# Kernel tuning notes

Measured on AMD Instinct MI355X. Metric: run time of the kernel, lower is better.

## Reference

```python
import jax, jax.numpy as jnp
import numpy as np

D_MODEL = 1024
N_HEADS = 16
D_HEAD = D_MODEL // N_HEADS
RANK = 16
DECAY = 0.95
ALPHA_MAX = 0.05
BETA = 0.01


def setup_inputs() -> dict:
    key = jax.random.key(0)
    ks = jax.random.split(key, 9)
    B, T = 4, 2048
    s = 0.02  # init scale for weights
    return {
        "hidden_states": jax.random.normal(ks[0], (B, T, D_MODEL), jnp.float32),
        "m_gate": jax.random.uniform(ks[1], (B, T), jnp.float32),
        "alpha_scale": jax.random.uniform(ks[2], (B, T, N_HEADS), jnp.float32),
        "Wq": jax.random.normal(ks[3], (D_MODEL, D_MODEL), jnp.float32) * s,
        "Wk": jax.random.normal(ks[4], (D_MODEL, D_MODEL), jnp.float32) * s,
        "Wv": jax.random.normal(ks[5], (D_MODEL, D_MODEL), jnp.float32) * s,
        "Wo": jax.random.normal(ks[6], (D_MODEL, D_MODEL), jnp.float32) * s,
        "Wa": jax.random.normal(ks[7], (N_HEADS, D_MODEL), jnp.float32) * s,
        "ba": jnp.zeros((N_HEADS,), jnp.float32),
        "mix_logit": jnp.zeros((N_HEADS,), jnp.float32),
    }


def reference(hidden_states, m_gate, alpha_scale, Wq, Wk, Wv, Wo, Wa, ba, mix_logit):
    B, T, D = hidden_states.shape
    H, Dh, R = N_HEADS, D_HEAD, RANK
    # batched projections (Linear: x @ W.T), then split heads
    q = (hidden_states @ Wq.T).reshape(B, T, H, Dh)
    k = (hidden_states @ Wk.T).reshape(B, T, H, Dh)
    v = (hidden_states @ Wv.T).reshape(B, T, H, Dh)
    # alpha computed under torch.no_grad in the original -> stop_gradient
    alpha = jax.nn.sigmoid(hidden_states @ Wa.T + ba)  # [B,T,H]
    alpha = alpha * m_gate[..., None] * alpha_scale
    alpha = jnp.minimum(alpha, ALPHA_MAX)
    alpha = jax.lax.stop_gradient(alpha)

    inv_sqrt_dh = 1.0 / (Dh ** 0.5)

    def step(carry, xs):
        U, V = carry  # U: [B,H,Dh,R], V: [B,H,R,Dh]
        q_t, k_t, v_t, a_t = xs  # [B,H,Dh], [B,H,Dh], [B,H,Dh], [B,H]
        U = DECAY * U
        V = DECAY * V
        ku = jnp.einsum('bhd,bhdr->bhr', k_t, U)
        a = a_t[..., None, None]
        U = U + a * jnp.einsum('bhd,bhr->bhdr', k_t, ku)
        V = V + a * jnp.einsum('bhr,bhd->bhrd', ku, v_t)
        U = U - BETA * jnp.clip(U, -1.0, 1.0)
        V = V - BETA * jnp.clip(V, -1.0, 1.0)
        # whole fast-weight update is no_grad in the original
        U = jax.lax.stop_gradient(U)
        V = jax.lax.stop_gradient(V)
        q_norm = q_t * inv_sqrt_dh
        k_fast = jnp.einsum('bhdr,bhrd->bhd', U, V)  # [B,H,Dh]
        score_slow = jnp.sum(q_norm * k_t, axis=-1)  # [B,H]
        score_fast = jnp.sum(q_norm * k_fast, axis=-1)
        logits = jnp.stack([score_slow, score_fast], axis=-1) + mix_logit[None, :, None]
        mix = jax.nn.softmax(logits, axis=-1)  # [B,H,2]
        y = mix[..., 0:1] * v_t + mix[..., 1:2] * k_fast  # [B,H,Dh]
        return (U, V), y

    U0 = jnp.zeros((B, H, Dh, R), hidden_states.dtype)
    V0 = jnp.zeros((B, H, R, Dh), hidden_states.dtype)
    xs = (jnp.moveaxis(q, 1, 0), jnp.moveaxis(k, 1, 0),
          jnp.moveaxis(v, 1, 0), jnp.moveaxis(alpha, 1, 0))
    _, ys = jax.lax.scan(step, (U0, V0), xs)  # ys: [T,B,H,Dh]
    y = jnp.moveaxis(ys, 0, 1).reshape(B, T, D)
    return y @ Wo.T
```

## Files before the change

kernel.cpp:

```cpp
#include <hip/hip_runtime.h>
#include <hip/hip_bf16.h>
#include <stdint.h>

#define D_MODEL 1024
#define N_HEADS 16
#define D_HEAD  64
#define SEQ_T   2048
#define BATCH   4

typedef unsigned short u16;
typedef __bf16 bf16x8 __attribute__((ext_vector_type(8)));
typedef float  f32x4  __attribute__((ext_vector_type(4)));

#define NT 32
#define BUF 4096

__device__ __forceinline__ u16 f2bf(float x) {
  unsigned u = __float_as_uint(x);
  u += 0x7fffu + ((u >> 16) & 1u);
  return (u16)(u >> 16);
}
__device__ __forceinline__ unsigned pk2(float a, float b) {
  return (unsigned)f2bf(a) | ((unsigned)f2bf(b) << 16);
}
__device__ __forceinline__ unsigned scale2(unsigned p, float s) {
  float lo = __uint_as_float(p << 16) * s;
  float hi = __uint_as_float(p & 0xffff0000u) * s;
  return pk2(lo, hi);
}
__device__ __forceinline__ void cp16(const u16* g, u16* l) {
  __builtin_amdgcn_global_load_lds(
      (const __attribute__((address_space(1))) unsigned int*)g,
      (__attribute__((address_space(3))) unsigned int*)l, 16, 0, 0);
}

__global__ __launch_bounds__(256) void cast_kernel(const float* __restrict__ hs,
                                                   const float* __restrict__ wq,
                                                   const float* __restrict__ wk,
                                                   const float* __restrict__ wv,
                                                   const float* __restrict__ wo,
                                                   u16* __restrict__ Xb,
                                                   u16* __restrict__ Wb) {
  int g = blockIdx.x * 256 + threadIdx.x;
  const float4* src; uint4* dst;
  if (g < (1 << 20)) {
    src = (const float4*)hs + 2 * (size_t)g;
    dst = (uint4*)Xb + g;
  } else {
    int j = g - (1 << 20);
    int R = j >> 7;
    int col8 = j & 127;
    const float* s;
    int srow;
    if (R < 2048) {
      int h = R >> 7, c = R & 127, jj = c >> 4, l = c & 15;
      srow = h * 64 + (jj >> 1) * 16 + l;
      s = (jj & 1) ? wk : wq;
    } else if (R < 3072) { s = wv; srow = R - 2048; }
    else                 { s = wo; srow = R - 3072; }
    src = (const float4*)s + (size_t)srow * 256 + col8 * 2;
    dst = (uint4*)Wb + (size_t)R * 128 + col8;
  }
  float4 lo = src[0], hi = src[1];
  uint4 o;
  o.x = pk2(lo.x, lo.y); o.y = pk2(lo.z, lo.w);
  o.z = pk2(hi.x, hi.y); o.w = pk2(hi.z, hi.w);
  *dst = o;
}

__global__ __launch_bounds__(256, 4) void gemm_qkv_kernel(const u16* __restrict__ A,
                                                          const u16* __restrict__ B,
                                                          u16* __restrict__ Vb,
                                                          float* __restrict__ S) {
  constexpr int K = D_MODEL;
  __shared__ u16 As[2 * BUF];
  __shared__ u16 Bs[2 * BUF];
  const int tid  = threadIdx.x;
  const int lane = tid & 63;
  const int wave = tid >> 6;
  const int wm = (wave >> 1) * 64;
  const int wn = (wave & 1) * 64;
  const int bm = blockIdx.y * 128;
  const int bn = blockIdx.x;
  const int quad = lane >> 4;
  const int l16  = lane & 15;
  const int rchunk = quad ^ ((l16 >> 1) & 3);

  const int lr = tid >> 2;
  const int lch = tid & 3;
  const int wch = lch ^ ((lr >> 1) & 3);
  const u16* Ap0 = A + (size_t)(bm + lr) * K + lch * 8;
  const u16* Ap1 = Ap0 + (size_t)64 * K;
  const u16* Bp0 = B + (size_t)(bn * 128 + lr) * K + lch * 8;
  const u16* Bp1 = Bp0 + (size_t)64 * K;
  u16* Aw0 = As + lr * 32 + wch * 8;
  u16* Aw1 = Aw0 + 64 * 32;
  u16* Bw0 = Bs + lr * 32 + wch * 8;
  u16* Bw1 = Bw0 + 64 * 32;

  f32x4 acc[4][4];
  #pragma unroll
  for (int i = 0; i < 4; ++i)
    #pragma unroll
    for (int j = 0; j < 4; ++j) acc[i][j] = (f32x4){0.f, 0.f, 0.f, 0.f};

  uint4 a0 = *(const uint4*)Ap0;
  uint4 a1 = *(const uint4*)Ap1;
  uint4 b0 = *(const uint4*)Bp0;
  uint4 b1 = *(const uint4*)Bp1;
  *(uint4*)Aw0 = a0; *(uint4*)Aw1 = a1;
  *(uint4*)Bw0 = b0; *(uint4*)Bw1 = b1;
  a0 = *(const uint4*)(Ap0 + 32);
  a1 = *(const uint4*)(Ap1 + 32);
  b0 = *(const uint4*)(Bp0 + 32);
  b1 = *(const uint4*)(Bp1 + 32);
  __syncthreads();

  #pragma unroll 2
  for (int t = 0; t < NT; ++t) {
    const int p = t & 1;
    const u16* Ar = As + p * BUF;
    const u16* Br = Bs + p * BUF;
    bf16x8 af[4], bfr[4];
    #pragma unroll
    for (int i = 0; i < 4; ++i)
      af[i] = *(const bf16x8*)(Ar + (wm + i * 16 + l16) * 32 + rchunk * 8);
    #pragma unroll
    for (int j = 0; j < 4; ++j)
      bfr[j] = *(const bf16x8*)(Br + (wn + j * 16 + l16) * 32 + rchunk * 8);
    if (t + 1 < NT) {
      const int q = (p ^ 1) * BUF;
      *(uint4*)(Aw0 + q) = a0; *(uint4*)(Aw1 + q) = a1;
      *(uint4*)(Bw0 + q) = b0; *(uint4*)(Bw1 + q) = b1;
      if (t + 2 < NT) {
        const int o = (t + 2) * 32;
        a0 = *(const uint4*)(Ap0 + o);
        a1 = *(const uint4*)(Ap1 + o);
        b0 = *(const uint4*)(Bp0 + o);
        b1 = *(const uint4*)(Bp1 + o);
      }
    }
    #pragma unroll
    for (int i = 0; i < 4; ++i)
      #pragma unroll
      for (int j = 0; j < 4; ++j)
        acc[i][j] = __builtin_amdgcn_mfma_f32_16x16x32_bf16(af[i], bfr[j], acc[i][j], 0, 0, 0);
    __syncthreads();
  }

  if (bn < N_HEADS) {
    float part[4][4];
    #pragma unroll
    for (int i = 0; i < 4; ++i)
      #pragma unroll
      for (int e = 0; e < 4; ++e)
        part[i][e] = acc[i][0][e] * acc[i][1][e] + acc[i][2][e] * acc[i][3][e];
    #pragma unroll
    for (int m = 1; m <= 8; m <<= 1)
      #pragma unroll
      for (int i = 0; i < 4; ++i)
        #pragma unroll
        for (int e = 0; e < 4; ++e)
          part[i][e] += __shfl_xor(part[i][e], m);
    __syncthreads();
    float* Sp = (float*)As;
    if (l16 == 0) {
      #pragma unroll
      for (int i = 0; i < 4; ++i)
        #pragma unroll
        for (int e = 0; e < 4; ++e)
          Sp[(wm + i * 16 + quad * 4 + e) * 2 + (wave & 1)] = part[i][e];
    }
    __syncthreads();
    if (tid < 128) {
      float s = (Sp[tid * 2] + Sp[tid * 2 + 1]) * 0.125f;
      S[(size_t)(bm + tid) * N_HEADS + bn] = 1.f / (1.f + __expf(-s));
    }
  } else {
    const int cb = (bn - N_HEADS) * 128;
    #pragma unroll
    for (int i = 0; i < 4; ++i)
      #pragma unroll
      for (int j = 0; j < 4; ++j)
        #pragma unroll
        for (int e = 0; e < 4; ++e) {
          int row = bm + wm + i * 16 + quad * 4 + e;
          int col = cb + wn + j * 16 + l16;
          Vb[(size_t)row * D_MODEL + col] = f2bf(acc[i][j][e]);
        }
  }
}

__global__ __launch_bounds__(256, 4) void gemm_out_kernel(const u16* __restrict__ A,
                                                          const u16* __restrict__ B,
                                                          const float* __restrict__ S,
                                                          float* __restrict__ C) {
  constexpr int K = D_MODEL, N = D_MODEL;
  __shared__ u16 As[2 * BUF];
  __shared__ u16 Bs[2 * BUF];
  const int tid  = threadIdx.x;
  const int lane = tid & 63;
  const int wave = tid >> 6;
  const int wm = (wave >> 1) * 64;
  const int wn = (wave & 1) * 64;
  const int bm = blockIdx.y * 128;
  const int bn = blockIdx.x * 128;
  const int quad = lane >> 4;
  const int l16  = lane & 15;
  const int rchunk = quad ^ ((l16 >> 1) & 3);

  const int lr = tid >> 2;
  const int lch = tid & 3;
  const int wch = lch ^ ((lr >> 1) & 3);
  const u16* Ap0 = A + (size_t)(bm + lr) * K + lch * 8;
  const u16* Ap1 = Ap0 + (size_t)64 * K;
  u16* Aw0 = As + lr * 32 + wch * 8;
  u16* Aw1 = Aw0 + 64 * 32;
  const float* Sp0 = S + (size_t)(bm + lr) * N_HEADS;
  const float* Sp1 = Sp0 + (size_t)64 * N_HEADS;

  const int srow = lane >> 2;
  const int gch  = (lane & 3) ^ ((lane >> 3) & 3);
  const u16* Bg0 = B + (size_t)(bn + wave * 16 + srow) * K + gch * 8;
  const u16* Bg1 = Bg0 + (size_t)64 * K;
  u16* Bl = Bs + wave * 16 * 32 + lane * 8;

  f32x4 acc[4][4];
  #pragma unroll
  for (int i = 0; i < 4; ++i)
    #pragma unroll
    for (int j = 0; j < 4; ++j) acc[i][j] = (f32x4){0.f, 0.f, 0.f, 0.f};

  uint4 a0 = *(const uint4*)Ap0;
  uint4 a1 = *(const uint4*)Ap1;
  float rs0 = Sp0[0], rs1 = Sp1[0];
  cp16(Bg0, Bl);           cp16(Bg1, Bl + 64 * 32);
  {
    uint4 w0, w1;
    w0.x = scale2(a0.x, rs0); w0.y = scale2(a0.y, rs0);
    w0.z = scale2(a0.z, rs0); w0.w = scale2(a0.w, rs0);
    w1.x = scale2(a1.x, rs1); w1.y = scale2(a1.y, rs1);
    w1.z = scale2(a1.z, rs1); w1.w = scale2(a1.w, rs1);
    *(uint4*)Aw0 = w0; *(uint4*)Aw1 = w1;
  }
  a0 = *(const uint4*)(Ap0 + 32);
  a1 = *(const uint4*)(Ap1 + 32);
  __syncthreads();

  #pragma unroll 2
  for (int t = 0; t < NT; ++t) {
    const int p = t & 1;
    const u16* Ar = As + p * BUF;
    const u16* Br = Bs + p * BUF;
    bf16x8 af[4], bfr[4];
    #pragma unroll
    for (int i = 0; i < 4; ++i)
      af[i] = *(const bf16x8*)(Ar + (wm + i * 16 + l16) * 32 + rchunk * 8);
    #pragma unroll
    for (int j = 0; j < 4; ++j)
      bfr[j] = *(const bf16x8*)(Br + (wn + j * 16 + l16) * 32 + rchunk * 8);
    if (t + 1 < NT) {
      const int q = (p ^ 1) * BUF;
      cp16(Bg0 + (t + 1) * 32, Bl + q);
      cp16(Bg1 + (t + 1) * 32, Bl + q + 64 * 32);
      uint4 w0, w1;
      w0.x = scale2(a0.x, rs0); w0.y = scale2(a0.y, rs0);
      w0.z = scale2(a0.z, rs0); w0.w = scale2(a0.w, rs0);
      w1.x = scale2(a1.x, rs1); w1.y = scale2(a1.y, rs1);
      w1.z = scale2(a1.z, rs1); w1.w = scale2(a1.w, rs1);
      *(uint4*)(Aw0 + q) = w0; *(uint4*)(Aw1 + q) = w1;
      if (t + 2 < NT) {
        const int o = (t + 2) * 32;
        a0 = *(const uint4*)(Ap0 + o);
        a1 = *(const uint4*)(Ap1 + o);
        rs0 = Sp0[(t + 2) >> 1];
        rs1 = Sp1[(t + 2) >> 1];
      }
    }
    #pragma unroll
    for (int i = 0; i < 4; ++i)
      #pragma unroll
      for (int j = 0; j < 4; ++j)
        acc[i][j] = __builtin_amdgcn_mfma_f32_16x16x32_bf16(af[i], bfr[j], acc[i][j], 0, 0, 0);
    __syncthreads();
  }

  #pragma unroll
  for (int i = 0; i < 4; ++i)
    #pragma unroll
    for (int j = 0; j < 4; ++j)
      #pragma unroll
      for (int e = 0; e < 4; ++e) {
        int row = bm + wm + i * 16 + quad * 4 + e;
        int col = bn + wn + j * 16 + l16;
        C[(size_t)row * N + col] = acc[i][j][e];
      }
}

extern "C" void kernel_launch(void* const* d_in, const int* in_sizes, int n_in,
                              void* d_out, int out_size, void* d_ws, size_t ws_size,
                              hipStream_t stream) {
  const float* hs = (const float*)d_in[0];
  const float* Wq = (const float*)d_in[3];
  const float* Wk = (const float*)d_in[4];
  const float* Wv = (const float*)d_in[5];
  const float* Wo = (const float*)d_in[6];

  char* ws = (char*)d_ws;
  u16*  Xb = (u16*)ws;
  u16*  Wb = (u16*)(ws + (16u << 20));
  u16*  Vb = (u16*)(ws + (24u << 20));
  float* Sb = (float*)(ws + (40u << 20));
  float* out = (float*)d_out;

  cast_kernel<<<6144, 256, 0, stream>>>(hs, Wq, Wk, Wv, Wo, Xb, Wb);
  gemm_qkv_kernel<<<dim3(24, 64), 256, 0, stream>>>(Xb, Wb, Vb, Sb);
  gemm_out_kernel<<<dim3(8, 64), 256, 0, stream>>>(
      Vb, Wb + (size_t)3072 * D_MODEL, Sb, out);
}
```

Baseline: 205.3 us.

## Rewrite QKV GEMM with 256x256 tiles, async LDS staging and 8-wave ping-pong schedule

```diff
diff --git a/kernel.cpp b/kernel.cpp
--- a/kernel.cpp
+++ b/kernel.cpp
@@ -68,125 +68,171 @@
   *dst = o;
 }
 
-__global__ __launch_bounds__(256, 4) void gemm_qkv_kernel(const u16* __restrict__ A,
+#define QLDA(buf, rq)                                                          \
+  do {                                                                         \
+    const u16* _p = Ls + (buf) * 32768 + (rq) * 8192 + wm * 4096 + l16 * 64;   \
+    _Pragma("unroll") for (int _i = 0; _i < 4; ++_i) {                         \
+      af[_i][0] = *(const bf16x8*)(_p + _i * 1024 + cA0);                      \
+      af[_i][1] = *(const bf16x8*)(_p + _i * 1024 + cA1);                      \
+    }                                                                          \
+  } while (0)
+#define QLDB(buf, cq)                                                          \
+  do {                                                                         \
+    const u16* _p = Ls + (buf) * 32768 + 16384 + (cq) * 8192 + wn * 2048 +     \
+                    l16 * 64;                                                  \
+    _Pragma("unroll") for (int _j = 0; _j < 2; ++_j) {                         \
+      bfr[_j][0] = *(const bf16x8*)(_p + _j * 1024 + cA0);                     \
+      bfr[_j][1] = *(const bf16x8*)(_p + _j * 1024 + cA1);                     \
+    }                                                                          \
+  } while (0)
+#define QMFMA(rq, cq)                                                          \
+  do {                                                                         \
+    __builtin_amdgcn_s_setprio(1);                                             \
+    _Pragma("unroll") for (int _i = 0; _i < 4; ++_i)                           \
+      _Pragma("unroll") for (int _j = 0; _j < 2; ++_j) {                       \
+        f32x4 _c = acc[(rq) * 4 + _i][(cq) * 2 + _j];                          \
+        _c = __builtin_amdgcn_mfma_f32_16x16x32_bf16(af[_i][0], bfr[_j][0],    \
+                                                     _c, 0, 0, 0);             \
+        _c = __builtin_amdgcn_mfma_f32_16x16x32_bf16(af[_i][1], bfr[_j][1],    \
+                                                     _c, 0, 0, 0);             \
+        acc[(rq) * 4 + _i][(cq) * 2 + _j] = _c;                                \
+      }                                                                        \
+    __builtin_amdgcn_s_setprio(0);                                             \
+  } while (0)
+#define QSTAGE_A(u, buf, t)                                                    \
+  do {                                                                         \
+    cp16(aSrc[u][0] + (t) * 64, dA + (buf) * 32768 + (u) * 8192);              \
+    cp16(aSrc[u][1] + (t) * 64, dA + (buf) * 32768 + (u) * 8192 + 512);        \
+  } while (0)
+#define QSTAGE_B(u, buf, t)                                                    \
+  do {                                                                         \
+    cp16(bSrc[u][0] + (t) * 64, dB + (buf) * 32768 + (u) * 8192);              \
+    cp16(bSrc[u][1] + (t) * 64, dB + (buf) * 32768 + (u) * 8192 + 512);        \
+  } while (0)
+#define QBAR()  __builtin_amdgcn_s_barrier()
+#define QWLGKM() asm volatile("s_waitcnt lgkmcnt(0)" ::: "memory")
+#define QWVM6() asm volatile("s_waitcnt vmcnt(6)" ::: "memory")
+#define QWVM0() asm volatile("s_waitcnt vmcnt(0)" ::: "memory")
+
+__global__ __launch_bounds__(512, 2) void gemm_qkv_kernel(const u16* __restrict__ A,
                                                           const u16* __restrict__ B,
                                                           u16* __restrict__ Vb,
                                                           float* __restrict__ S) {
-  constexpr int K = D_MODEL;
-  __shared__ u16 As[2 * BUF];
-  __shared__ u16 Bs[2 * BUF];
+  __shared__ u16 Ls[65536];
   const int tid  = threadIdx.x;
-  const int lane = tid & 63;
-  const int wave = tid >> 6;
-  const int wm = (wave >> 1) * 64;
-  const int wn = (wave & 1) * 64;
-  const int bm = blockIdx.y * 128;
-  const int bn = blockIdx.x;
-  const int quad = lane >> 4;
-  const int l16  = lane & 15;
-  const int rchunk = quad ^ ((l16 >> 1) & 3);
-
-  const int lr = tid >> 2;
-  const int lch = tid & 3;
-  const int wch = lch ^ ((lr >> 1) & 3);
-  const u16* Ap0 = A + (size_t)(bm + lr) * K + lch * 8;
-  const u16* Ap1 = Ap0 + (size_t)64 * K;
-  const u16* Bp0 = B + (size_t)(bn * 128 + lr) * K + lch * 8;
-  const u16* Bp1 = Bp0 + (size_t)64 * K;
-  u16* Aw0 = As + lr * 32 + wch * 8;
-  u16* Aw1 = Aw0 + 64 * 32;
-  u16* Bw0 = Bs + lr * 32 + wch * 8;
-  u16* Bw1 = Bw0 + 64 * 32;
-
-  f32x4 acc[4][4];
+  const int w    = tid >> 6;
+  const int l    = tid & 63;
+  const int quad = l >> 4;
+  const int l16  = l & 15;
+  const int wm   = w >> 2;
+  const int wn   = w & 3;
+  const int bn   = blockIdx.x;
+  const int bm   = blockIdx.y;
+
+  const int rl0  = w * 16 + (l >> 3);
+  const int rl1  = rl0 + 8;
+  const int csrc = ((l & 7) ^ (l >> 3)) * 8;
+  const u16* aSrc[2][2];
+  const u16* bSrc[2][2];
   #pragma unroll
-  for (int i = 0; i < 4; ++i)
+  for (int u = 0; u < 2; ++u) {
+    int ra0 = (rl0 >> 6) * 128 + u * 64 + (rl0 & 63);
+    int ra1 = (rl1 >> 6) * 128 + u * 64 + (rl1 & 63);
+    aSrc[u][0] = A + (size_t)(bm * 256 + ra0) * 1024 + csrc;
+    aSrc[u][1] = A + (size_t)(bm * 256 + ra1) * 1024 + csrc;
+    int cb0 = (rl0 >> 5) * 64 + u * 32 + (rl0 & 31);
+    int cb1 = (rl1 >> 5) * 64 + u * 32 + (rl1 & 31);
+    bSrc[u][0] = B + (size_t)(bn * 256 + cb0) * 1024 + csrc;
+    bSrc[u][1] = B + (size_t)(bn * 256 + cb1) * 1024 + csrc;
+  }
+  u16* dA = Ls + w * 1024 + l * 8;
+  u16* dB = dA + 16384;
+
+  const int cA0 = ((0 * 4 + quad) ^ (l16 & 7)) * 8;
+  const int cA1 = ((1 * 4 + quad) ^ (l16 & 7)) * 8;
+
+  f32x4 acc[8][4];
+  #pragma unroll
+  for (int i = 0; i < 8; ++i)
     #pragma unroll
     for (int j = 0; j < 4; ++j) acc[i][j] = (f32x4){0.f, 0.f, 0.f, 0.f};
-
-  uint4 a0 = *(const uint4*)Ap0;
-  uint4 a1 = *(const uint4*)Ap1;
-  uint4 b0 = *(const uint4*)Bp0;
-  uint4 b1 = *(const uint4*)Bp1;
-  *(uint4*)Aw0 = a0; *(uint4*)Aw1 = a1;
-  *(uint4*)Bw0 = b0; *(uint4*)Bw1 = b1;
-  a0 = *(const uint4*)(Ap0 + 32);
-  a1 = *(const uint4*)(Ap1 + 32);
-  b0 = *(const uint4*)(Bp0 + 32);
-  b1 = *(const uint4*)(Bp1 + 32);
-  __syncthreads();
-
-  #pragma unroll 2
-  for (int t = 0; t < NT; ++t) {
-    const int p = t & 1;
-    const u16* Ar = As + p * BUF;
-    const u16* Br = Bs + p * BUF;
-    bf16x8 af[4], bfr[4];
-    #pragma unroll
-    for (int i = 0; i < 4; ++i)
-      af[i] = *(const bf16x8*)(Ar + (wm + i * 16 + l16) * 32 + rchunk * 8);
-    #pragma unroll
-    for (int j = 0; j < 4; ++j)
-      bfr[j] = *(const bf16x8*)(Br + (wn + j * 16 + l16) * 32 + rchunk * 8);
-    if (t + 1 < NT) {
-      const int q = (p ^ 1) * BUF;
-      *(uint4*)(Aw0 + q) = a0; *(uint4*)(Aw1 + q) = a1;
-      *(uint4*)(Bw0 + q) = b0; *(uint4*)(Bw1 + q) = b1;
-      if (t + 2 < NT) {
-        const int o = (t + 2) * 32;
-        a0 = *(const uint4*)(Ap0 + o);
-        a1 = *(const uint4*)(Ap1 + o);
-        b0 = *(const uint4*)(Bp0 + o);
-        b1 = *(const uint4*)(Bp1 + o);
-      }
-    }
-    #pragma unroll
-    for (int i = 0; i < 4; ++i)
-      #pragma unroll
-      for (int j = 0; j < 4; ++j)
-        acc[i][j] = __builtin_amdgcn_mfma_f32_16x16x32_bf16(af[i], bfr[j], acc[i][j], 0, 0, 0);
-    __syncthreads();
-  }
-
-  if (bn < N_HEADS) {
-    float part[4][4];
-    #pragma unroll
-    for (int i = 0; i < 4; ++i)
+  bf16x8 af[4][2], bfr[2][2];
+
+  QSTAGE_A(0, 0, 0); QSTAGE_A(1, 0, 0); QSTAGE_B(0, 0, 0); QSTAGE_B(1, 0, 0);
+  QSTAGE_A(0, 1, 1); QSTAGE_A(1, 1, 1); QSTAGE_B(0, 1, 1); QSTAGE_B(1, 1, 1);
+  QWVM0();
+  QBAR();
+
+  #pragma unroll 1
+  for (int j = 0; j < 8; ++j) {
+    const int tE = 2 * j + 2, tO = 2 * j + 3;
+    QLDA(0, 0); QLDB(0, 0);
+    if (j > 0) QSTAGE_B(0, 1, 2 * j + 1);
+    QBAR(); QWLGKM(); QMFMA(0, 0); QBAR();
+    QLDB(0, 1);
+    if (j < 7) QSTAGE_A(0, 0, tE);
+    QBAR(); QWLGKM(); QMFMA(0, 1); QBAR();
+    QLDA(0, 1);
+    if (j < 7) QSTAGE_B(1, 0, tE);
+    QBAR(); QWLGKM(); QMFMA(1, 1); QBAR();
+    QLDB(0, 0);
+    if (j < 7) { QSTAGE_A(1, 0, tE); QWVM6(); } else { QWVM0(); }
+    QBAR(); QWLGKM(); QMFMA(1, 0); QBAR();
+    QLDA(1, 0); QLDB(1, 0);
+    if (j < 7) QSTAGE_B(0, 0, tE);
+    QBAR(); QWLGKM(); QMFMA(0, 0); QBAR();
+    QLDB(1, 1);
+    if (j < 7) QSTAGE_A(0, 1, tO);
+    QBAR(); QWLGKM(); QMFMA(0, 1); QBAR();
+    QLDA(1, 1);
+    if (j < 7) QSTAGE_B(1, 1, tO);
+    QBAR(); QWLGKM(); QMFMA(1, 1); QBAR();
+    QLDB(1, 0);
+    if (j < 7) QSTAGE_A(1, 1, tO);
+    QWVM6();
+    QBAR(); QWLGKM(); QMFMA(1, 0); QBAR();
+  }
+
+  if (bn < 8) {
+    float part[8][4];
+    #pragma unroll
+    for (int fr = 0; fr < 8; ++fr)
       #pragma unroll
       for (int e = 0; e < 4; ++e)
-        part[i][e] = acc[i][0][e] * acc[i][1][e] + acc[i][2][e] * acc[i][3][e];
+        part[fr][e] = acc[fr][0][e] * acc[fr][1][e] + acc[fr][2][e] * acc[fr][3][e];
     #pragma unroll
     for (int m = 1; m <= 8; m <<= 1)
       #pragma unroll
-      for (int i = 0; i < 4; ++i)
+      for (int fr = 0; fr < 8; ++fr)
         #pragma unroll
         for (int e = 0; e < 4; ++e)
-          part[i][e] += __shfl_xor(part[i][e], m);
-    __syncthreads();
-    float* Sp = (float*)As;
+          part[fr][e] += __shfl_xor(part[fr][e], m);
+    float* Sp = (float*)Ls;
     if (l16 == 0) {
       #pragma unroll
-      for (int i = 0; i < 4; ++i)
+      for (int fr = 0; fr < 8; ++fr)
         #pragma unroll
         for (int e = 0; e < 4; ++e)
-          Sp[(wm + i * 16 + quad * 4 + e) * 2 + (wave & 1)] = part[i][e];
+          Sp[(wm * 128 + fr * 16 + quad * 4 + e) * 4 + wn] = part[fr][e];
     }
     __syncthreads();
-    if (tid < 128) {
-      float s = (Sp[tid * 2] + Sp[tid * 2 + 1]) * 0.125f;
-      S[(size_t)(bm + tid) * N_HEADS + bn] = 1.f / (1.f + __expf(-s));
+    {
+      int h = tid >> 8, row = tid & 255;
+      float s = (Sp[row * 4 + h * 2] + Sp[row * 4 + h * 2 + 1]) * 0.125f;
+      S[(size_t)(bm * 256 + row) * N_HEADS + bn * 2 + h] =
+          1.f / (1.f + __expf(-s));
     }
   } else {
-    const int cb = (bn - N_HEADS) * 128;
-    #pragma unroll
-    for (int i = 0; i < 4; ++i)
-      #pragma unroll
-      for (int j = 0; j < 4; ++j)
+    const int cb = (bn - 8) * 256;
+    #pragma unroll
+    for (int fr = 0; fr < 8; ++fr)
+      #pragma unroll
+      for (int ci = 0; ci < 4; ++ci)
         #pragma unroll
         for (int e = 0; e < 4; ++e) {
-          int row = bm + wm + i * 16 + quad * 4 + e;
-          int col = cb + wn + j * 16 + l16;
-          Vb[(size_t)row * D_MODEL + col] = f2bf(acc[i][j][e]);
+          int row = bm * 256 + wm * 128 + fr * 16 + quad * 4 + e;
+          int col = cb + wn * 64 + ci * 16 + l16;
+          Vb[(size_t)row * D_MODEL + col] = f2bf(acc[fr][ci][e]);
         }
   }
 }
@@ -314,7 +360,7 @@
   float* out = (float*)d_out;
 
   cast_kernel<<<6144, 256, 0, stream>>>(hs, Wq, Wk, Wv, Wo, Xb, Wb);
-  gemm_qkv_kernel<<<dim3(24, 64), 256, 0, stream>>>(Xb, Wb, Vb, Sb);
+  gemm_qkv_kernel<<<dim3(12, 32), 512, 0, stream>>>(Xb, Wb, Vb, Sb);
   gemm_out_kernel<<<dim3(8, 64), 256, 0, stream>>>(
       Vb, Wb + (size_t)3072 * D_MODEL, Sb, out);
 }
```

Result: no change. 206.8 us (+0.7%).
